# Performance work log

Hardware: AMD Instinct MI355X
Metric: run time of the kernel (lower is better)

## Reference

```python
import jax, jax.numpy as jnp
import numpy as np

B, F, O = 32, 26, 20
IN, G = 2048, 512
REL = 53
EPS = 1e-5  # BatchNorm1d default eps


def setup_inputs() -> dict:
    key = jax.random.key(0)
    ks = jax.random.split(key, 10)
    inp = {
        "region_feats": jax.random.normal(ks[0], (B, F, O, IN), jnp.float32),
        "region_masks": jnp.ones((B, F, O), jnp.float32),
        "rel_feats": jax.random.randint(ks[1], (B, F, O, O), 0, REL, jnp.int64),
        "tem_feats": jax.random.uniform(ks[2], (B, F * O, F * O), jnp.float32),
        # learned params (eval mode: dropout off, BN uses running stats)
        "rel_W": jax.random.normal(ks[3], (G, IN), jnp.float32) * (1.0 / np.sqrt(IN)),
        "rel_b": jnp.zeros((G,), jnp.float32),
        "rel_emb": jax.random.normal(ks[4], (REL, G), jnp.float32) * 0.02,
        "tem_W": jax.random.normal(ks[5], (G, IN), jnp.float32) * (1.0 / np.sqrt(IN)),
        "tem_b": jnp.zeros((G,), jnp.float32),
        "bn_w": jnp.ones((F * O,), jnp.float32),
        "bn_b": jnp.zeros((F * O,), jnp.float32),
        "bn_rm": jnp.zeros((F * O,), jnp.float32),
        "bn_rv": jnp.ones((F * O,), jnp.float32),
    }
    return inp


def reference(region_feats, region_masks, rel_feats, tem_feats,
              rel_W, rel_b, rel_emb, tem_W, tem_b,
              bn_w, bn_b, bn_rm, bn_rv):
    b, f, o, _ = region_feats.shape
    # ---- RELATIONAL FEATURE GRAPH ----
    # [B,F,O,G]
    rel_region = jnp.einsum("bfoi,gi->bfog", region_feats, rel_W) + rel_b
    # embedding lookup: [B,F,O,O,G]
    emb = rel_emb[rel_feats]
    mask = (rel_feats > 0).astype(region_feats.dtype)  # [B,F,O,O]
    msum = jnp.sum(mask, axis=3)                        # [B,F,O]
    # sum_j mask_ij * emb_ij  (masked reduction over neighbor dim)
    emb_sum = jnp.einsum("bfijg,bfij->bfig", emb, mask)
    # sum_j mask_ij * r_i == r_i * msum_i, so (emb_sum + r*msum)/msum
    rel_out = (emb_sum + rel_region * msum[..., None]) / msum[..., None]
    rel_out = rel_out.reshape(b, f * o, -1)
    # ---- TEMPORAL FEATURE GRAPH ----
    tem_region = jnp.einsum("bfoi,gi->bfog", region_feats, tem_W) + tem_b
    tem_region = tem_region.reshape(b, f * o, -1)
    tem_sum = jnp.sum(tem_feats, axis=2)                # [B, F*O]
    tem_out = jnp.matmul(tem_feats, tem_region) / tem_sum[..., None]
    # ---- OUTPUT ----
    out = jnp.concatenate([rel_out, tem_out], axis=-1)  # [B, F*O, 2G]
    out = jnp.tanh(out)
    # BatchNorm1d over channel dim 1 (eval mode, running stats)
    inv = bn_w / jnp.sqrt(bn_rv + EPS)                  # [F*O]
    out = (out - bn_rm[None, :, None]) * inv[None, :, None] + bn_b[None, :, None]
    return out
```

## Files before the change

### kernel.cpp

```cpp
#include <hip/hip_runtime.h>
#include <stdint.h>

#define BB 32
#define FO 520
#define M1 16640
#define KIN 2048
#define KA 2112
#define N1 1024
#define GG 512
#define K2P 576
#define M2 640

typedef unsigned short u16;
typedef short v8s __attribute__((ext_vector_type(8)));
typedef float v4f __attribute__((ext_vector_type(4)));

__device__ __forceinline__ u16 f2bf(float f) {
  union { float f; unsigned u; } v; v.f = f;
  unsigned r = v.u + 0x7fffu + ((v.u >> 16) & 1u);
  return (u16)(r >> 16);
}

__device__ __forceinline__ float fast_tanh(float x) {
  float cx = fminf(fmaxf(x, -15.f), 15.f);
  float e = __expf(2.f * cx);
  return (e - 1.f) / (e + 1.f);
}

__device__ __forceinline__ void glds(const u16* g, u16* l) {
  __builtin_amdgcn_global_load_lds((const __attribute__((address_space(1))) void*)g,
                                   (__attribute__((address_space(3))) void*)l, 16, 0, 0);
}

#define PREP_ROWS 8832
__global__ __launch_bounds__(512) void prep_all_kernel(
    const float* __restrict__ rf, const int* __restrict__ rel,
    const float* __restrict__ relW, const float* __restrict__ temW,
    const float* __restrict__ emb, const float* __restrict__ tem,
    u16* __restrict__ A1, u16* __restrict__ Wc,
    u16* __restrict__ A2, float* __restrict__ tsum) {
  const int blk = blockIdx.x;
  const int t = threadIdx.x;
  if (blk < PREP_ROWS) {
    const int row = blk * 2 + (t >> 8);
    const int tt = t & 255;
    const float* src;
    u16* orow;
    if (row < M1) { src = rf + (size_t)row * KIN; orow = A1 + (size_t)row * KA; }
    else {
      const int n = row - M1;
      src = (n < GG) ? (relW + (size_t)n * KIN) : (temW + (size_t)(n - GG) * KIN);
      orow = Wc + (size_t)n * KA;
    }
    const v4f* p = (const v4f*)src;
    v4f a = __builtin_nontemporal_load(p + 2 * tt);
    v4f b = __builtin_nontemporal_load(p + 2 * tt + 1);
    v8s v;
    v[0] = (short)f2bf(a[0]); v[1] = (short)f2bf(a[1]);
    v[2] = (short)f2bf(a[2]); v[3] = (short)f2bf(a[3]);
    v[4] = (short)f2bf(b[0]); v[5] = (short)f2bf(b[1]);
    v[6] = (short)f2bf(b[2]); v[7] = (short)f2bf(b[3]);
    *(v8s*)(orow + tt * 8) = v;
    if (tt < 64) {
      float sval = 0.f;
      if (row < M1) {
        const int* rp = rel + (size_t)row * 20;
        int cnt = 0, ms = 0;
#pragma unroll
        for (int j = 0; j < 20; ++j) { int ix = rp[j]; cnt += (ix == tt + 1); ms += (ix > 0); }
        if (tt < 52 && ms > 0) sval = (float)cnt / (float)ms;
      } else {
        const int n = row - M1;
        if (n < GG && tt < 52) sval = emb[(size_t)(tt + 1) * GG + n];
      }
      orow[KIN + tt] = f2bf(sval);
    }
    return;
  }
  const int w = t >> 6, l = t & 63;
  const int row = (blk - PREP_ROWS) * 8 + w;
  const int b = row / M2, i = row % M2;
  u16* orow = A2 + (size_t)row * K2P;
  v8s z = {0, 0, 0, 0, 0, 0, 0, 0};
  if (i >= FO) {
    *(v8s*)(orow + l * 8) = z;
    if (l < 8) *(v8s*)(orow + (64 + l) * 8) = z;
    return;
  }
  const float* srow = tem + ((size_t)b * FO + i) * FO;
  float s = 0.f;
  {
    v4f a = __builtin_nontemporal_load((const v4f*)(srow + 8 * l));
    v4f bb = __builtin_nontemporal_load((const v4f*)(srow + 8 * l + 4));
    s += a[0] + a[1] + a[2] + a[3] + bb[0] + bb[1] + bb[2] + bb[3];
    v8s v;
    v[0] = (short)f2bf(a[0]); v[1] = (short)f2bf(a[1]);
    v[2] = (short)f2bf(a[2]); v[3] = (short)f2bf(a[3]);
    v[4] = (short)f2bf(bb[0]); v[5] = (short)f2bf(bb[1]);
    v[6] = (short)f2bf(bb[2]); v[7] = (short)f2bf(bb[3]);
    *(v8s*)(orow + l * 8) = v;
  }
  if (l < 8) {
    if (l == 0) {
      v4f a = __builtin_nontemporal_load((const v4f*)(srow + 512));
      v4f bb = __builtin_nontemporal_load((const v4f*)(srow + 516));
      s += a[0] + a[1] + a[2] + a[3] + bb[0] + bb[1] + bb[2] + bb[3];
      v8s v;
      v[0] = (short)f2bf(a[0]); v[1] = (short)f2bf(a[1]);
      v[2] = (short)f2bf(a[2]); v[3] = (short)f2bf(a[3]);
      v[4] = (short)f2bf(bb[0]); v[5] = (short)f2bf(bb[1]);
      v[6] = (short)f2bf(bb[2]); v[7] = (short)f2bf(bb[3]);
      *(v8s*)(orow + 512) = v;
    } else {
      *(v8s*)(orow + (64 + l) * 8) = z;
    }
  }
#pragma unroll
  for (int off = 32; off > 0; off >>= 1) s += __shfl_down(s, off);
  if (l == 0) tsum[(size_t)b * FO + i] = s;
}

template <int G>
__device__ __forceinline__ void gemm1_body(
    const u16* __restrict__ A, const u16* __restrict__ Wc,
    const float* __restrict__ rel_b, const float* __restrict__ tem_b,
    const float* __restrict__ bn_w, const float* __restrict__ bn_b,
    const float* __restrict__ bn_rm, const float* __restrict__ bn_rv,
    float* __restrict__ out, u16* __restrict__ BT, u16* smem,
    const int m0, const int n0) {
  constexpr int SB = (G + 1) * 4096;
  const int tid = threadIdx.x;
  const int lane = tid & 63;
  const int wv = tid >> 6, wm = wv >> 1, wn = wv & 1;
  const int quad = lane >> 4, r16 = lane & 15;

  const u16 *ga0, *ga1 = nullptr, *gb0;
  {
    const int r0 = tid >> 2, sl0 = tid & 3;
    const int c0 = (sl0 ^ ((r0 >> 1) & 3)) * 8;
    ga0 = A + (size_t)(m0 + r0) * KA + c0;
    if constexpr (G == 2) ga1 = A + (size_t)(m0 + 128 + r0) * KA + c0;
    gb0 = Wc + (size_t)(n0 + r0) * KA + c0;
  }
  const int lofA0 = wv * 512;
  const int lofA1 = 4096 + wv * 512;
  const int lofB0 = G * 4096 + wv * 512;

  auto STAGE = [&](int dstoff) {
    u16* dst_ = smem + dstoff;
    glds(ga0, dst_ + lofA0);
    if constexpr (G == 2) { glds(ga1, dst_ + lofA1); ga1 += 32; }
    glds(gb0, dst_ + lofB0);
    ga0 += 32; gb0 += 32;
  };

  v4f acc[2 * G][4];
#pragma unroll
  for (int i = 0; i < 2 * G; ++i)
#pragma unroll
    for (int j = 0; j < 4; ++j) { v4f z = {0.f, 0.f, 0.f, 0.f}; acc[i][j] = z; }

  auto COMPUTE = [&](int cbuf) {
    const u16* As_ = smem + cbuf * SB;
    const u16* Bs_ = As_ + G * 4096;
    v8s af[2 * G], bf[4];
#pragma unroll
    for (int i = 0; i < 2 * G; ++i) {
      const int ra = wm * (G * 32) + i * 16 + r16;
      af[i] = *(const v8s*)&As_[ra * 32 + ((quad ^ ((ra >> 1) & 3)) * 8)];
    }
#pragma unroll
    for (int j = 0; j < 4; ++j) {
      const int rb = wn * 64 + j * 16 + r16;
      bf[j] = *(const v8s*)&Bs_[rb * 32 + ((quad ^ ((rb >> 1) & 3)) * 8)];
    }
#pragma unroll
    for (int i = 0; i < 2 * G; ++i)
#pragma unroll
      for (int j = 0; j < 4; ++j)
        acc[i][j] = __builtin_amdgcn_mfma_f32_16x16x32_bf16(af[i], bf[j], acc[i][j], 0, 0, 0);
  };

  STAGE(0);
  STAGE(SB);

  int cb = 0, nb = 2;
  for (int t = 0; t < 64; ++t) {
    STAGE(nb * SB);
    if constexpr (G == 2) asm volatile("s_waitcnt vmcnt(6)" ::: "memory");
    else                  asm volatile("s_waitcnt vmcnt(4)" ::: "memory");
    __builtin_amdgcn_s_barrier();
    COMPUTE(cb);
    asm volatile("s_waitcnt lgkmcnt(0)" ::: "memory");
    __builtin_amdgcn_s_barrier();
    cb = (cb == 2) ? 0 : cb + 1;
    nb = (nb == 2) ? 0 : nb + 1;
  }
  {
    const int cb1 = (cb == 2) ? 0 : cb + 1;
    if constexpr (G == 2) asm volatile("s_waitcnt vmcnt(3)" ::: "memory");
    else                  asm volatile("s_waitcnt vmcnt(2)" ::: "memory");
    __builtin_amdgcn_s_barrier();
    COMPUTE(cb);
    asm volatile("s_waitcnt vmcnt(0) lgkmcnt(0)" ::: "memory");
    __builtin_amdgcn_s_barrier();
    COMPUTE(cb1);
  }

  if (n0 < GG) {
#pragma unroll
    for (int mtt = 0; mtt < 2 * G; ++mtt) {
      const int mb = m0 + wm * (G * 32) + mtt * 16 + quad * 4;
      const int bb = mb / FO;
      const int fo0 = mb - bb * FO;
      float inv[4], rm[4], bofs[4];
#pragma unroll
      for (int r = 0; r < 4; ++r) {
        const int fo = fo0 + r;
        inv[r] = bn_w[fo] * rsqrtf(bn_rv[fo] + 1e-5f);
        rm[r] = bn_rm[fo]; bofs[r] = bn_b[fo];
      }
#pragma unroll
      for (int ntt = 0; ntt < 4; ++ntt) {
        const int n = n0 + wn * 64 + ntt * 16 + r16;
        const float rbn = rel_b[n];
#pragma unroll
        for (int r = 0; r < 4; ++r) {
          float val = (fast_tanh(acc[mtt][ntt][r] + rbn) - rm[r]) * inv[r] + bofs[r];
          __builtin_nontemporal_store(val, out + (size_t)(mb + r) * N1 + n);
        }
      }
    }
  } else {
    constexpr int SP = G * 128 + 8;
    __syncthreads();
#pragma unroll
    for (int p = 0; p < 2; ++p) {
      if (p) __syncthreads();
      if (wn == p) {
#pragma unroll
        for (int mtt = 0; mtt < 2 * G; ++mtt) {
          const int il = wm * (G * 32) + mtt * 16 + quad * 4;
#pragma unroll
          for (int ntt = 0; ntt < 4; ++ntt) {
            const int gl = ntt * 16 + r16;
            const float tb = tem_b[(n0 - GG) + p * 64 + gl];
            ushort4 w;
            w.x = f2bf(acc[mtt][ntt][0] + tb);
            w.y = f2bf(acc[mtt][ntt][1] + tb);
            w.z = f2bf(acc[mtt][ntt][2] + tb);
            w.w = f2bf(acc[mtt][ntt][3] + tb);
            *(ushort4*)&smem[gl * SP + il] = w;
          }
        }
      }
      __syncthreads();
      if constexpr (G == 2) {
#pragma unroll
        for (int pass = 0; pass < 4; ++pass) {
          const int gl = pass * 16 + (tid >> 5);
          const int ch = tid & 31;
          const int m = m0 + ch * 8;
          const int b1 = m / FO;
          const int i1 = m - b1 * FO;
          v8s val = *(const v8s*)&smem[gl * SP + ch * 8];
          const int g = (n0 - GG) + p * 64 + gl;
          *(v8s*)(BT + ((size_t)(b1 * GG + g)) * K2P + i1) = val;
        }
      } else {
#pragma unroll
        for (int pass = 0; pass < 2; ++pass) {
          const int gl = pass * 32 + (tid >> 4);
          const int ch = tid & 15;
          const int m = m0 + ch * 8;
          const int b1 = m / FO;
          const int i1 = m - b1 * FO;
          v8s val = *(const v8s*)&smem[gl * SP + ch * 8];
          const int g = (n0 - GG) + p * 64 + gl;
          *(v8s*)(BT + ((size_t)(b1 * GG + g)) * K2P + i1) = val;
        }
      }
    }
  }
}

__global__ __launch_bounds__(512, 4) void gemm1_kernel(
    const u16* __restrict__ A, const u16* __restrict__ Wc,
    const float* __restrict__ rel_b, const float* __restrict__ tem_b,
    const float* __restrict__ bn_w, const float* __restrict__ bn_b,
    const float* __restrict__ bn_rm, const float* __restrict__ bn_rv,
    float* __restrict__ out, u16* __restrict__ BT) {
  __shared__ u16 smem[36864];
  const int id = blockIdx.x;
  if (id < 512) {
    const int wgid = (id & 7) * 64 + (id >> 3);
    gemm1_body<2>(A, Wc, rel_b, tem_b, bn_w, bn_b, bn_rm, bn_rv, out, BT, smem,
                  (wgid >> 3) * 256, (wgid & 7) * 128);
  } else {
    const int sid = id - 512;
    gemm1_body<1>(A, Wc, rel_b, tem_b, bn_w, bn_b, bn_rm, bn_rv, out, BT, smem,
                  16384 + (sid >> 3) * 128, (sid & 7) * 128);
  }
}

#define G2_STAGE(DST)                                                                            \
  do {                                                                                           \
    u16* dst_ = smem + (DST);                                                                    \
    glds(ga0, dst_ + lofA0); glds(gb0, dst_ + lofB0); glds(gb1, dst_ + lofB1);                   \
    ga0 += 32; gb0 += 32; gb1 += 32;                                                             \
  } while (0)

#define G2_COMPUTE(CB)                                                                           \
  do {                                                                                           \
    const u16* As_ = smem + (CB) * 12288;                                                        \
    const u16* Bs_ = As_ + 4096;                                                                 \
    v8s af[4], bf[4];                                                                            \
    _Pragma("unroll") for (int t4 = 0; t4 < 4; ++t4) {                                           \
      const int ra = wm * 64 + t4 * 16 + r16;                                                    \
      const int rb = wn * 64 + t4 * 16 + r16;                                                    \
      af[t4] = *(const v8s*)&As_[ra * 32 + ((quad ^ ((ra >> 1) & 3)) * 8)];                      \
      bf[t4] = *(const v8s*)&Bs_[rb * 32 + ((quad ^ ((rb >> 1) & 3)) * 8)];                      \
    }                                                                                            \
    _Pragma("unroll") for (int mtt = 0; mtt < 4; ++mtt)                                          \
      _Pragma("unroll") for (int ntt = 0; ntt < 4; ++ntt)                                        \
        acc[mtt][ntt] =                                                                          \
            __builtin_amdgcn_mfma_f32_16x16x32_bf16(af[mtt], bf[ntt], acc[mtt][ntt], 0, 0, 0);   \
  } while (0)

__global__ __launch_bounds__(512, 4) void gemm2_kernel(
    const u16* __restrict__ A2, const u16* __restrict__ BT,
    const float* __restrict__ tsum,
    const float* __restrict__ bn_w, const float* __restrict__ bn_b,
    const float* __restrict__ bn_rm, const float* __restrict__ bn_rv,
    float* __restrict__ out) {
  __shared__ u16 smem[36864];
  const int tid = threadIdx.x;
  const int lane = tid & 63;
  const int wv = tid >> 6, wm = wv >> 2, wn = wv & 3;
  const int m0 = blockIdx.x * 128;
  const int n0 = blockIdx.y * 256;
  const int b = blockIdx.z;
  const u16* Ab = A2 + (size_t)b * M2 * K2P;
  const u16* Bb = BT + (size_t)b * GG * K2P;
  const int quad = lane >> 4, r16 = lane & 15;

  const u16 *ga0, *gb0, *gb1;
  {
    const int r0 = tid >> 2, sl0 = tid & 3;
    const int c0 = (sl0 ^ ((r0 >> 1) & 3)) * 8;
    ga0 = Ab + (size_t)(m0 + r0) * K2P + c0;
    gb0 = Bb + (size_t)(n0 + r0) * K2P + c0;
    gb1 = Bb + (size_t)(n0 + 128 + r0) * K2P + c0;
  }
  const int lofA0 = wv * 512;
  const int lofB0 = 4096 + wv * 512;
  const int lofB1 = 8192 + wv * 512;

  v4f acc[4][4];
#pragma unroll
  for (int i = 0; i < 4; ++i)
#pragma unroll
    for (int j = 0; j < 4; ++j) { v4f z = {0.f, 0.f, 0.f, 0.f}; acc[i][j] = z; }

  G2_STAGE(0);
  G2_STAGE(12288);

  int cb = 0, nb = 2;
  for (int t = 0; t < 16; ++t) {
    G2_STAGE(nb * 12288);
    asm volatile("s_waitcnt vmcnt(6)" ::: "memory");
    __builtin_amdgcn_s_barrier();
    G2_COMPUTE(cb);
    asm volatile("s_waitcnt lgkmcnt(0)" ::: "memory");
    __builtin_amdgcn_s_barrier();
    cb = (cb == 2) ? 0 : cb + 1;
    nb = (nb == 2) ? 0 : nb + 1;
  }
  {
    const int cb1 = (cb == 2) ? 0 : cb + 1;
    asm volatile("s_waitcnt vmcnt(3)" ::: "memory");
    __builtin_amdgcn_s_barrier();
    G2_COMPUTE(cb);
    asm volatile("s_waitcnt vmcnt(0) lgkmcnt(0)" ::: "memory");
    __builtin_amdgcn_s_barrier();
    G2_COMPUTE(cb1);
  }

#pragma unroll
  for (int mtt = 0; mtt < 4; ++mtt) {
    const int ibase = m0 + wm * 64 + mtt * 16 + quad * 4;
    if (ibase >= FO) continue;
    float ts[4], inv[4], rm[4], bofs[4];
#pragma unroll
    for (int r = 0; r < 4; ++r) {
      const int i = ibase + r;
      ts[r] = 1.f / tsum[(size_t)b * FO + i];
      inv[r] = bn_w[i] * rsqrtf(bn_rv[i] + 1e-5f);
      rm[r] = bn_rm[i]; bofs[r] = bn_b[i];
    }
#pragma unroll
    for (int ntt = 0; ntt < 4; ++ntt) {
      const int g = n0 + wn * 64 + ntt * 16 + r16;
#pragma unroll
      for (int r = 0; r < 4; ++r) {
        float val = (fast_tanh(acc[mtt][ntt][r] * ts[r]) - rm[r]) * inv[r] + bofs[r];
        __builtin_nontemporal_store(val, out + ((size_t)(b * FO + (ibase + r))) * N1 + GG + g);
      }
    }
  }
}

extern "C" void kernel_launch(void* const* d_in, const int* in_sizes, int n_in,
                              void* d_out, int out_size, void* d_ws, size_t ws_size,
                              hipStream_t stream) {
  const float* region_feats = (const float*)d_in[0];
  const int* rel_feats = (const int*)d_in[2];
  const float* tem_feats = (const float*)d_in[3];
  const float* rel_W = (const float*)d_in[4];
  const float* rel_b = (const float*)d_in[5];
  const float* rel_emb = (const float*)d_in[6];
  const float* tem_W = (const float*)d_in[7];
  const float* tem_b = (const float*)d_in[8];
  const float* bn_w = (const float*)d_in[9];
  const float* bn_b = (const float*)d_in[10];
  const float* bn_rm = (const float*)d_in[11];
  const float* bn_rv = (const float*)d_in[12];
  float* out = (float*)d_out;

  char* base = (char*)d_ws;
  u16* A1 = (u16*)base;
  u16* Wc = (u16*)(base + 70287360);
  u16* A2 = (u16*)(base + 74612736);
  u16* BT = (u16*)(base + 98205696);
  float* tsum = (float*)(base + 117080064);

  prep_all_kernel<<<PREP_ROWS + 2560, 512, 0, stream>>>(
      region_feats, rel_feats, rel_W, tem_W, rel_emb, tem_feats, A1, Wc, A2, tsum);
  gemm1_kernel<<<528, 512, 0, stream>>>(A1, Wc, rel_b, tem_b,
                                        bn_w, bn_b, bn_rm, bn_rv, out, BT);
  gemm2_kernel<<<dim3(5, 2, 32), 512, 0, stream>>>(A2, BT, tsum,
                                                   bn_w, bn_b, bn_rm, bn_rv, out);
}
```

Baseline: 375.5 us.

## Split-K the gemm1 tail tiles and reduce them in a finish kernel

The 16 leftover 128x128 tail tiles of the first GEMM are split six ways along K (352 columns each). That gives 96 blocks writing fp32 partial sums to workspace instead of 16 full-K blocks. A new finish kernel sums the partials and applies the bias, tanh and BatchNorm epilogue, or the bf16 transpose into BT. This targets the long tail where a few blocks ran the whole K loop after the main tiles finished. It costs an extra kernel launch plus partial-sum traffic, and it only runs when the workspace is large enough.

```diff
diff --git a/kernel.cpp b/kernel.cpp
--- a/kernel.cpp
+++ b/kernel.cpp
@@ -284,22 +284,199 @@
   }
 }
 
+__device__ __forceinline__ void gemm1_partial(
+    const u16* __restrict__ A, const u16* __restrict__ Wc,
+    float* __restrict__ pb, u16* smem, const int m0, const int n0, const int k0) {
+  constexpr int SB = 8192;
+  const int tid = threadIdx.x;
+  const int lane = tid & 63;
+  const int wv = tid >> 6, wm = wv >> 1, wn = wv & 1;
+  const int quad = lane >> 4, r16 = lane & 15;
+
+  const u16 *ga0, *gb0;
+  {
+    const int r0 = tid >> 2, sl0 = tid & 3;
+    const int c0 = (sl0 ^ ((r0 >> 1) & 3)) * 8;
+    ga0 = A + (size_t)(m0 + r0) * KA + k0 + c0;
+    gb0 = Wc + (size_t)(n0 + r0) * KA + k0 + c0;
+  }
+  const int lofA0 = wv * 512;
+  const int lofB0 = 4096 + wv * 512;
+
+  auto STAGE = [&](int dstoff) {
+    u16* dst_ = smem + dstoff;
+    glds(ga0, dst_ + lofA0);
+    glds(gb0, dst_ + lofB0);
+    ga0 += 32; gb0 += 32;
+  };
+
+  v4f acc[2][4];
+#pragma unroll
+  for (int i = 0; i < 2; ++i)
+#pragma unroll
+    for (int j = 0; j < 4; ++j) { v4f z = {0.f, 0.f, 0.f, 0.f}; acc[i][j] = z; }
+
+  auto COMPUTE = [&](int cbuf) {
+    const u16* As_ = smem + cbuf * SB;
+    const u16* Bs_ = As_ + 4096;
+    v8s af[2], bf[4];
+#pragma unroll
+    for (int i = 0; i < 2; ++i) {
+      const int ra = wm * 32 + i * 16 + r16;
+      af[i] = *(const v8s*)&As_[ra * 32 + ((quad ^ ((ra >> 1) & 3)) * 8)];
+    }
+#pragma unroll
+    for (int j = 0; j < 4; ++j) {
+      const int rb = wn * 64 + j * 16 + r16;
+      bf[j] = *(const v8s*)&Bs_[rb * 32 + ((quad ^ ((rb >> 1) & 3)) * 8)];
+    }
+#pragma unroll
+    for (int i = 0; i < 2; ++i)
+#pragma unroll
+      for (int j = 0; j < 4; ++j)
+        acc[i][j] = __builtin_amdgcn_mfma_f32_16x16x32_bf16(af[i], bf[j], acc[i][j], 0, 0, 0);
+  };
+
+  STAGE(0);
+  STAGE(SB);
+  int cb = 0, nb = 2;
+  for (int t = 0; t < 9; ++t) {
+    STAGE(nb * SB);
+    asm volatile("s_waitcnt vmcnt(4)" ::: "memory");
+    __builtin_amdgcn_s_barrier();
+    COMPUTE(cb);
+    asm volatile("s_waitcnt lgkmcnt(0)" ::: "memory");
+    __builtin_amdgcn_s_barrier();
+    cb = (cb == 2) ? 0 : cb + 1;
+    nb = (nb == 2) ? 0 : nb + 1;
+  }
+  {
+    const int cb1 = (cb == 2) ? 0 : cb + 1;
+    asm volatile("s_waitcnt vmcnt(2)" ::: "memory");
+    __builtin_amdgcn_s_barrier();
+    COMPUTE(cb);
+    asm volatile("s_waitcnt vmcnt(0) lgkmcnt(0)" ::: "memory");
+    __builtin_amdgcn_s_barrier();
+    COMPUTE(cb1);
+  }
+
+#pragma unroll
+  for (int mtt = 0; mtt < 2; ++mtt)
+#pragma unroll
+    for (int ntt = 0; ntt < 4; ++ntt)
+      *(v4f*)(pb + ((size_t)((wv * 2 + mtt) * 4 + ntt)) * 256 + lane * 4) = acc[mtt][ntt];
+}
+
 __global__ __launch_bounds__(512, 4) void gemm1_kernel(
     const u16* __restrict__ A, const u16* __restrict__ Wc,
     const float* __restrict__ rel_b, const float* __restrict__ tem_b,
     const float* __restrict__ bn_w, const float* __restrict__ bn_b,
     const float* __restrict__ bn_rm, const float* __restrict__ bn_rv,
-    float* __restrict__ out, u16* __restrict__ BT) {
+    float* __restrict__ out, u16* __restrict__ BT,
+    float* __restrict__ partial, const int splitk) {
   __shared__ u16 smem[36864];
   const int id = blockIdx.x;
   if (id < 512) {
     const int wgid = (id & 7) * 64 + (id >> 3);
     gemm1_body<2>(A, Wc, rel_b, tem_b, bn_w, bn_b, bn_rm, bn_rv, out, BT, smem,
                   (wgid >> 3) * 256, (wgid & 7) * 128);
+  } else if (splitk) {
+    const int sid = id - 512;
+    const int tile = sid & 15, split = sid >> 4;
+    gemm1_partial(A, Wc, partial + ((size_t)(split * 16 + tile)) * 16384, smem,
+                  16384 + (tile >> 3) * 128, (tile & 7) * 128, split * 352);
   } else {
     const int sid = id - 512;
     gemm1_body<1>(A, Wc, rel_b, tem_b, bn_w, bn_b, bn_rm, bn_rv, out, BT, smem,
                   16384 + (sid >> 3) * 128, (sid & 7) * 128);
+  }
+}
+
+__global__ __launch_bounds__(512) void tail_finish_kernel(
+    const float* __restrict__ partial,
+    const float* __restrict__ rel_b, const float* __restrict__ tem_b,
+    const float* __restrict__ bn_w, const float* __restrict__ bn_b,
+    const float* __restrict__ bn_rm, const float* __restrict__ bn_rv,
+    float* __restrict__ out, u16* __restrict__ BT) {
+  __shared__ u16 smem[64 * 136];
+  const int s = blockIdx.x;
+  const int m0 = 16384 + (s >> 3) * 128, n0 = (s & 7) * 128;
+  const int tid = threadIdx.x;
+  const int lane = tid & 63;
+  const int wv = tid >> 6, wm = wv >> 1, wn = wv & 1;
+  const int quad = lane >> 4, r16 = lane & 15;
+
+  v4f acc[2][4];
+  const float* pb = partial + (size_t)s * 16384;
+#pragma unroll
+  for (int mtt = 0; mtt < 2; ++mtt)
+#pragma unroll
+    for (int ntt = 0; ntt < 4; ++ntt) {
+      const size_t fo = ((size_t)((wv * 2 + mtt) * 4 + ntt)) * 256 + lane * 4;
+      v4f a = *(const v4f*)(pb + fo);
+#pragma unroll
+      for (int k = 1; k < 6; ++k) a += *(const v4f*)(pb + (size_t)k * 262144 + fo);
+      acc[mtt][ntt] = a;
+    }
+
+  if (n0 < GG) {
+#pragma unroll
+    for (int mtt = 0; mtt < 2; ++mtt) {
+      const int mb = m0 + wm * 32 + mtt * 16 + quad * 4;
+      const int bb = mb / FO;
+      const int fo0 = mb - bb * FO;
+      float inv[4], rm[4], bofs[4];
+#pragma unroll
+      for (int r = 0; r < 4; ++r) {
+        const int fo = fo0 + r;
+        inv[r] = bn_w[fo] * rsqrtf(bn_rv[fo] + 1e-5f);
+        rm[r] = bn_rm[fo]; bofs[r] = bn_b[fo];
+      }
+#pragma unroll
+      for (int ntt = 0; ntt < 4; ++ntt) {
+        const int n = n0 + wn * 64 + ntt * 16 + r16;
+        const float rbn = rel_b[n];
+#pragma unroll
+        for (int r = 0; r < 4; ++r) {
+          float val = (fast_tanh(acc[mtt][ntt][r] + rbn) - rm[r]) * inv[r] + bofs[r];
+          __builtin_nontemporal_store(val, out + (size_t)(mb + r) * N1 + n);
+        }
+      }
+    }
+  } else {
+#pragma unroll
+    for (int p = 0; p < 2; ++p) {
+      if (p) __syncthreads();
+      if (wn == p) {
+#pragma unroll
+        for (int mtt = 0; mtt < 2; ++mtt) {
+          const int il = wm * 32 + mtt * 16 + quad * 4;
+#pragma unroll
+          for (int ntt = 0; ntt < 4; ++ntt) {
+            const int gl = ntt * 16 + r16;
+            const float tb = tem_b[(n0 - GG) + p * 64 + gl];
+            ushort4 w;
+            w.x = f2bf(acc[mtt][ntt][0] + tb);
+            w.y = f2bf(acc[mtt][ntt][1] + tb);
+            w.z = f2bf(acc[mtt][ntt][2] + tb);
+            w.w = f2bf(acc[mtt][ntt][3] + tb);
+            *(ushort4*)&smem[gl * 136 + il] = w;
+          }
+        }
+      }
+      __syncthreads();
+#pragma unroll
+      for (int pass = 0; pass < 2; ++pass) {
+        const int gl = pass * 32 + (tid >> 4);
+        const int ch = tid & 15;
+        const int m = m0 + ch * 8;
+        const int b1 = m / FO;
+        const int i1 = m - b1 * FO;
+        v8s val = *(const v8s*)&smem[gl * 136 + ch * 8];
+        const int g = (n0 - GG) + p * 64 + gl;
+        *(v8s*)(BT + ((size_t)(b1 * GG + g)) * K2P + i1) = val;
+      }
+    }
   }
 }
 
@@ -433,11 +610,17 @@
   u16* A2 = (u16*)(base + 74612736);
   u16* BT = (u16*)(base + 98205696);
   float* tsum = (float*)(base + 117080064);
+  float* partial = (float*)(base + 117146624);
+  const int splitk = (ws_size >= 123438080u) ? 1 : 0;
 
   prep_all_kernel<<<PREP_ROWS + 2560, 512, 0, stream>>>(
       region_feats, rel_feats, rel_W, tem_W, rel_emb, tem_feats, A1, Wc, A2, tsum);
-  gemm1_kernel<<<528, 512, 0, stream>>>(A1, Wc, rel_b, tem_b,
-                                        bn_w, bn_b, bn_rm, bn_rv, out, BT);
+  gemm1_kernel<<<splitk ? 608 : 528, 512, 0, stream>>>(A1, Wc, rel_b, tem_b,
+                                                       bn_w, bn_b, bn_rm, bn_rv, out, BT,
+                                                       partial, splitk);
+  if (splitk)
+    tail_finish_kernel<<<16, 512, 0, stream>>>(partial, rel_b, tem_b,
+                                               bn_w, bn_b, bn_rm, bn_rv, out, BT);
   gemm2_kernel<<<dim3(5, 2, 32), 512, 0, stream>>>(A2, BT, tsum,
                                                    bn_w, bn_b, bn_rm, bn_rv, out);
 }
```

Result: no change. 373.3 us (-0.6%).
